# Kernel optimization log

Measured on AMD Instinct MI355X. Metric: run time of the kernel, lower is better.

## Reference

```python
import jax, jax.numpy as jnp
import numpy as np

CLS_W, BBOX_W, GIOU_W = 1.0, 5.0, 2.0
EPS = 1e-6


def _cxcywh_to_xyxy(b):
    cx, cy, w, h = b[..., 0], b[..., 1], b[..., 2], b[..., 3]
    return jnp.stack((cx - 0.5 * w, cy - 0.5 * h, cx + 0.5 * w, cy + 0.5 * h), axis=-1)


def _pairwise_giou(b1, b2):
    # b1: [N,4] xyxy, b2: [M,4] xyxy -> [N,M]
    b1 = b1[:, None, :]
    b2 = b2[None, :, :]
    iw = jnp.clip(jnp.minimum(b1[..., 2], b2[..., 2]) - jnp.maximum(b1[..., 0], b2[..., 0]), 0.0)
    ih = jnp.clip(jnp.minimum(b1[..., 3], b2[..., 3]) - jnp.maximum(b1[..., 1], b2[..., 1]), 0.0)
    inter = iw * ih
    area1 = (b1[..., 2] - b1[..., 0]) * (b1[..., 3] - b1[..., 1])
    area2 = (b2[..., 2] - b2[..., 0]) * (b2[..., 3] - b2[..., 1])
    union = area1 + area2 - inter
    iou = inter / (union + EPS)
    enc = (jnp.maximum(b1[..., 2], b2[..., 2]) - jnp.minimum(b1[..., 0], b2[..., 0])) * \
          (jnp.maximum(b1[..., 3], b2[..., 3]) - jnp.minimum(b1[..., 1], b2[..., 1])) + EPS
    return iou - (enc - union) / enc


def _cost_single(logits, boxes, tids, tboxes):
    # logits [N,C], boxes [N,4] cxcywh, tids [M] int, tboxes [M,4] cxcywh
    prob = jax.nn.softmax(logits, axis=-1)          # [N,C]
    cost_cls = -prob[:, tids]                        # [N,M] (num_classes>1: no id shift)
    cost_bbox = jnp.sum(jnp.abs(boxes[:, None, :] - tboxes[None, :, :]), axis=-1)  # L1 cdist
    giou = _pairwise_giou(_cxcywh_to_xyxy(boxes), _cxcywh_to_xyxy(tboxes))
    return CLS_W * cost_cls + BBOX_W * cost_bbox + GIOU_W * (-giou)


_batched_cost = jax.jit(jax.vmap(_cost_single))


def _lsa(cost):
    """Jonker-Volgenant style Hungarian, equivalent to scipy.linear_sum_assignment."""
    cost = np.asarray(cost, dtype=np.float64)
    transposed = cost.shape[0] > cost.shape[1]
    if transposed:
        cost = cost.T
    n, m = cost.shape
    INF = 1e18
    u = np.zeros(n + 1)
    v = np.zeros(m + 1)
    p = np.zeros(m + 1, dtype=np.int64)   # p[j] = row (1-based) matched to col j
    way = np.zeros(m + 1, dtype=np.int64)
    for i in range(1, n + 1):
        p[0] = i
        j0 = 0
        minv = np.full(m + 1, INF)
        used = np.zeros(m + 1, dtype=bool)
        while True:
            used[j0] = True
            i0 = p[j0]
            free = ~used[1:]
            cur = cost[i0 - 1] - u[i0] - v[1:]
            upd = free & (cur < minv[1:])
            minv[1:] = np.where(upd, cur, minv[1:])
            way[1:] = np.where(upd, j0, way[1:])
            cand = np.where(free, minv[1:], INF)
            j1 = int(np.argmin(cand)) + 1
            delta = cand[j1 - 1]
            u[p[used]] += delta
            v[used] -= delta
            minv[1:] = np.where(free, minv[1:] - delta, minv[1:])
            j0 = j1
            if p[j0] == 0:
                break
        while j0:
            j1 = way[j0]
            p[j0] = p[j1]
            j0 = j1
    col4row = np.zeros(n, dtype=np.int64)
    for j in range(1, m + 1):
        if p[j] > 0:
            col4row[p[j] - 1] = j - 1
    if transposed:
        order = np.argsort(col4row, kind='stable').astype(np.int64)
        return col4row[order], order
    return np.arange(n, dtype=np.int64), col4row


def setup_inputs() -> dict:
    key = jax.random.key(0)
    k1, k2, k3, k4 = jax.random.split(key, 4)
    B, N, C, M = 64, 900, 91, 128
    return {
        "pred_logits": jax.random.normal(k1, (B, N, C), dtype=jnp.float32),
        "pred_boxes": jax.random.uniform(k2, (B, N, 4), dtype=jnp.float32),
        "tgt_labels": jax.random.randint(k3, (B, M), 0, C, dtype=jnp.int64),
        "tgt_boxes": jax.random.uniform(k4, (B, M, 4), dtype=jnp.float32),
    }


def reference(pred_logits, pred_boxes, tgt_labels, tgt_boxes):
    # Batched cost matrix on accelerator, then per-image assignment on host
    C = _batched_cost(pred_logits, pred_boxes, tgt_labels, tgt_boxes)  # [B,N,M]
    Cn = np.asarray(C)
    rows, cols = [], []
    for b in range(Cn.shape[0]):
        r, c = _lsa(Cn[b])
        rows.append(r)
        cols.append(c)
    return jnp.asarray(np.stack(rows)), jnp.asarray(np.stack(cols))
```

## Files before the change

kernel.cpp:

```cpp
#include <hip/hip_runtime.h>
#include <hip/hip_bf16.h>
#include <float.h>

#define BB 64
#define NN 900
#define CC 91
#define MM 128
#define BIG 1e18
#define DINF __builtin_huge_val()
#define NSLOT 15
#define LAST_VALID 4
#define TPB_C 128

__global__ __launch_bounds__(TPB_C) void cost_kernel(
    const float* __restrict__ logits,
    const float* __restrict__ boxes,
    const int*   __restrict__ tlabels,
    const float* __restrict__ tboxes,
    float* __restrict__ costT)
{
    const int b   = blockIdx.y;
    const int p0  = blockIdx.x * TPB_C;
    const int cnt = min(TPB_C, NN - p0);
    const int tid = threadIdx.x;

    __shared__ float s_lg[TPB_C * CC];
    __shared__ float s_tb[MM][4];
    __shared__ int   s_tl[MM];

    {
        s_tl[tid] = tlabels[b * MM + tid];
        const float4 tb4 = ((const float4*)tboxes)[(size_t)b * MM + tid];
        s_tb[tid][0] = tb4.x; s_tb[tid][1] = tb4.y;
        s_tb[tid][2] = tb4.z; s_tb[tid][3] = tb4.w;
    }
    {
        const float* gbase = logits + ((size_t)b * NN + p0) * CC;
        const int total = cnt * CC;
        const int n4 = total >> 2;
        for (int k = tid; k < n4; k += TPB_C)
            ((float4*)s_lg)[k] = ((const float4*)gbase)[k];
        for (int k = (n4 << 2) + tid; k < total; k += TPB_C)
            s_lg[k] = gbase[k];
    }
    __syncthreads();
    if (tid >= cnt) return;

    const float* lg = s_lg + tid * CC;
    float mx = -INFINITY;
    for (int c = 0; c < CC; ++c) mx = fmaxf(mx, lg[c]);
    float ssum = 0.f;
    for (int c = 0; c < CC; ++c) ssum += expf(lg[c] - mx);

    const float4 bx4 = ((const float4*)boxes)[(size_t)b * NN + p0 + tid];
    const float cx = bx4.x, cy = bx4.y, w = bx4.z, h = bx4.w;
    const float px0 = cx - 0.5f * w, py0 = cy - 0.5f * h;
    const float px1 = cx + 0.5f * w, py1 = cy + 0.5f * h;
    const float parea = (px1 - px0) * (py1 - py0);

    float* outp = costT + (size_t)b * MM * NN + p0 + tid;
    for (int j = 0; j < MM; ++j) {
        const float tcx = s_tb[j][0], tcy = s_tb[j][1], tw = s_tb[j][2], th = s_tb[j][3];
        float l1 = ((fabsf(cx - tcx) + fabsf(cy - tcy)) + fabsf(w - tw)) + fabsf(h - th);
        const float tx0 = tcx - 0.5f * tw, ty0 = tcy - 0.5f * th;
        const float tx1 = tcx + 0.5f * tw, ty1 = tcy + 0.5f * th;
        float iw = fminf(px1, tx1) - fmaxf(px0, tx0); iw = fmaxf(iw, 0.f);
        float ih = fminf(py1, ty1) - fmaxf(py0, ty0); ih = fmaxf(ih, 0.f);
        const float inter = iw * ih;
        const float tarea = (tx1 - tx0) * (ty1 - ty0);
        const float uni   = parea + tarea - inter;
        const float iou   = inter / (uni + 1e-6f);
        const float enc   = (fmaxf(px1, tx1) - fminf(px0, tx0)) *
                            (fmaxf(py1, ty1) - fminf(py0, ty0)) + 1e-6f;
        const float giou  = iou - (enc - uni) / enc;
        const float pcls  = expf(lg[s_tl[j]] - mx) / ssum;
        const float cost  = (1.0f * (-pcls) + 5.0f * l1) + 2.0f * (-giou);
        outp[(size_t)j * NN] = cost;
    }
}

template<int CTRL, int ROW_MASK>
__device__ __forceinline__ unsigned dpp_min_u32_step(unsigned x) {
    const unsigned m = (unsigned)__builtin_amdgcn_update_dpp((int)x, (int)x, CTRL, ROW_MASK, 0xF, false);
    return m < x ? m : x;
}
__device__ __forceinline__ unsigned wave_min_u32(unsigned x) {
    x = dpp_min_u32_step<0xB1,  0xF>(x);
    x = dpp_min_u32_step<0x4E,  0xF>(x);
    x = dpp_min_u32_step<0x141, 0xF>(x);
    x = dpp_min_u32_step<0x140, 0xF>(x);
    x = dpp_min_u32_step<0x142, 0xA>(x);
    x = dpp_min_u32_step<0x143, 0xC>(x);
    return (unsigned)__builtin_amdgcn_readlane((int)x, 63);
}
__device__ __forceinline__ int d_hi(double d) { return (int)(__double_as_longlong(d) >> 32); }
__device__ __forceinline__ int d_lo(double d) { return (int)__double_as_longlong(d); }
__device__ __forceinline__ double mk_d(int hi, int lo) {
    return __longlong_as_double(((long long)hi << 32) | (unsigned long long)(unsigned)lo);
}

__global__ __launch_bounds__(64) void lsa_kernel(
    const float* __restrict__ costT,
    int* __restrict__ out)
{
    const int b    = blockIdx.x;
    const int lane = threadIdx.x;

    __shared__ double s_u[MM + 1];
    __shared__ int    s_p[NN + 1];
    __shared__ int    s_c4r[MM];
    __shared__ int    s_spill[3 * (NN + 2)];

    double v[NSLOT], minv[NSLOT];
    unsigned pay[NSLOT], pay_base[NSLOT];
    float  cv[NSLOT];

    for (int j = lane; j <= NN; j += 64) s_p[j] = 0;
    for (int i = lane; i <= MM; i += 64) s_u[i] = 0.0;
    #pragma unroll
    for (int s = 0; s < NSLOT; ++s) {
        v[s] = 0.0;
        pay_base[s] = ((unsigned)(s * 64 + lane + 1) << 18);
        pay[s] = pay_base[s];
    }
    __syncthreads();

    const float* cb = costT + (size_t)b * MM * NN;

    #pragma unroll
    for (int s = 0; s < NSLOT; ++s) {
        const bool valid = (s < NSLOT - 1) || (lane < LAST_VALID);
        cv[s] = valid ? cb[s * 64 + lane] : 0.f;
    }

    for (int i = 1; i <= MM; ++i) {
        unsigned used_mask = 0;
        #pragma unroll
        for (int s = 0; s < NSLOT; ++s) minv[s] = BIG;

        int T = 0;
        int curj0 = 0;
        int curi0 = i;
        int curway = 0;
        int nspill = 0;
        double ui0 = 0.0;
        int my_j0 = -1, my_i0 = 0, my_way = 0;

        while (true) {
            if (T < 63) {
                if (lane == T) { my_j0 = curj0; my_i0 = curi0; my_way = curway; }
            } else {
                if (lane == 0) {
                    s_spill[3 * nspill]     = curj0;
                    s_spill[3 * nspill + 1] = curi0;
                    s_spill[3 * nspill + 2] = curway;
                }
                ++nspill;
            }
            if (curj0 > 0) {
                const int jp = curj0 - 1;
                if ((jp & 63) == lane) used_mask |= 1u << (jp >> 6);
            }

            const unsigned pay_or = (unsigned)curj0 << 8;
            #pragma unroll
            for (int s = 0; s < NSLOT; ++s) {
                const bool valid = (s < NSLOT - 1) || (lane < LAST_VALID);
                const bool fr = valid && !((used_mask >> s) & 1u);
                const double cur = ((double)cv[s] - ui0) - v[s];
                const bool imp = fr && (cur < minv[s]);
                if (imp) { minv[s] = cur; pay[s] = pay_base[s] | pay_or; }
            }

            double n1v[8]; unsigned n1p[8];
            #pragma unroll
            for (int s = 0; s < 8; ++s) {
                const int a = 2 * s, c = 2 * s + 1;
                double va = minv[a]; unsigned pa = pay[a];
                if (c < NSLOT) { if (minv[c] < va) { va = minv[c]; pa = pay[c]; } }
                n1v[s] = va; n1p[s] = pa;
            }
            double n2v[4]; unsigned n2p[4];
            #pragma unroll
            for (int s = 0; s < 4; ++s) {
                double va = n1v[2*s]; unsigned pa = n1p[2*s];
                if (n1v[2*s+1] < va) { va = n1v[2*s+1]; pa = n1p[2*s+1]; }
                n2v[s] = va; n2p[s] = pa;
            }
            double n3v[2]; unsigned n3p[2];
            #pragma unroll
            for (int s = 0; s < 2; ++s) {
                double va = n2v[2*s]; unsigned pa = n2p[2*s];
                if (n2v[2*s+1] < va) { va = n2v[2*s+1]; pa = n2p[2*s+1]; }
                n3v[s] = va; n3p[s] = pa;
            }
            double bv = n3v[0]; unsigned bpay = n3p[0];
            if (n3v[1] < bv) { bv = n3v[1]; bpay = n3p[1]; }

            const double bvn = bv + 0.0;
            const int hi = d_hi(bvn);
            const int sm = hi >> 31;
            const unsigned th = (unsigned)(hi ^ (sm | 0x80000000));
            const unsigned minhi = wave_min_u32(th);

            const unsigned long long hit = __ballot(th == minhi);
            unsigned wpay; double delta;
            if (__builtin_popcountll(hit) == 1) {
                const int src = (int)__builtin_ctzll(hit);
                wpay  = (unsigned)__builtin_amdgcn_readlane((int)bpay, src);
                delta = mk_d(__builtin_amdgcn_readlane(hi, src),
                             __builtin_amdgcn_readlane(d_lo(bvn), src));
            } else {
                const unsigned tl = (unsigned)(d_lo(bvn) ^ sm);
                const unsigned minlo = wave_min_u32((th == minhi) ? tl : 0xFFFFFFFFu);
                const bool full = (th == minhi) && (tl == minlo);
                wpay = wave_min_u32(full ? bpay : 0xFFFFFFFFu);
                const int src = (int)__builtin_ctzll(__ballot(full));
                delta = mk_d(__builtin_amdgcn_readlane(hi, src),
                             __builtin_amdgcn_readlane(d_lo(bvn), src));
            }
            const int j1   = (int)(wpay >> 18);
            const int way1 = (int)((wpay >> 8) & 0x3FF);
            const int pj1  = (int)(wpay & 0xFF);

            double ui_next = 0.0;
            if (pj1 != 0) {
                const float* crow = cb + (size_t)(pj1 - 1) * NN;
                #pragma unroll
                for (int s = 0; s < NSLOT; ++s) {
                    const bool valid = (s < NSLOT - 1) || (lane < LAST_VALID);
                    if (valid) cv[s] = crow[s * 64 + lane];
                }
                ui_next = s_u[pj1];
            }

            if (T < 63) {
                if (lane <= T) s_u[my_i0] += delta;
            } else {
                if (lane == 0) s_u[i] += delta;
                double uval[NSLOT];
                #pragma unroll
                for (int s = 0; s < NSLOT; ++s) {
                    const bool valid = (s < NSLOT - 1) || (lane < LAST_VALID);
                    if (valid && ((used_mask >> s) & 1u))
                        uval[s] = s_u[pay_base[s] & 0xFF];
                }
                #pragma unroll
                for (int s = 0; s < NSLOT; ++s) {
                    const bool valid = (s < NSLOT - 1) || (lane < LAST_VALID);
                    if (valid && ((used_mask >> s) & 1u))
                        s_u[pay_base[s] & 0xFF] = uval[s] + delta;
                }
            }
            #pragma unroll
            for (int s = 0; s < NSLOT; ++s) {
                const bool valid = (s < NSLOT - 1) || (lane < LAST_VALID);
                if (valid) {
                    const bool ub = (used_mask >> s) & 1u;
                    v[s]    = ub ? v[s] - delta : v[s];
                    minv[s] = ub ? DINF : minv[s] - delta;
                }
            }

            if (pj1 == 0) {
                int ja = j1, jb = way1;
                const int cap = (T < 63) ? T : 62;
                while (jb != 0) {
                    int np, nw;
                    const unsigned long long bal = __ballot(lane <= cap && my_j0 == jb);
                    if (bal != 0) {
                        const int src = (int)__builtin_ctzll(bal);
                        np = __builtin_amdgcn_readlane(my_i0, src);
                        nw = __builtin_amdgcn_readlane(my_way, src);
                    } else {
                        np = 0; nw = 0;
                        for (int k = 0; k < nspill; ++k) {
                            if (s_spill[3 * k] == jb) {
                                np = s_spill[3 * k + 1];
                                nw = s_spill[3 * k + 2];
                                break;
                            }
                        }
                    }
                    if (lane == 0) s_p[ja] = np;
                    ja = jb; jb = nw;
                }
                if (lane == 0) s_p[ja] = i;
                break;
            }
            curj0 = j1; curi0 = pj1; curway = way1; ui0 = ui_next; ++T;
        }

        #pragma unroll
        for (int s = 0; s < NSLOT; ++s) {
            const bool valid = (s < NSLOT - 1) || (lane < LAST_VALID);
            if (valid) {
                const int j = s * 64 + lane + 1;
                pay_base[s] = ((unsigned)j << 18) | (unsigned)s_p[j];
            }
        }
        if (i < MM) {
            const float* crow = cb + (size_t)i * NN;
            #pragma unroll
            for (int s = 0; s < NSLOT; ++s) {
                const bool valid = (s < NSLOT - 1) || (lane < LAST_VALID);
                if (valid) cv[s] = crow[s * 64 + lane];
            }
        }
    }

    for (int j = 1 + lane; j <= NN; j += 64) {
        const int pj = s_p[j];
        if (pj > 0) s_c4r[pj - 1] = j - 1;
    }
    __syncthreads();

    for (int t = lane; t < MM; t += 64) {
        const int val = s_c4r[t];
        int rank = 0;
        for (int q = 0; q < MM; ++q) rank += (s_c4r[q] < val);
        out[(size_t)b * MM + rank] = val;
        out[(size_t)BB * MM + (size_t)b * MM + rank] = t;
    }
}

extern "C" void kernel_launch(void* const* d_in, const int* in_sizes, int n_in,
                              void* d_out, int out_size, void* d_ws, size_t ws_size,
                              hipStream_t stream) {
    const float* logits  = (const float*)d_in[0];
    const float* boxes   = (const float*)d_in[1];
    const int*   tlabels = (const int*)d_in[2];
    const float* tboxes  = (const float*)d_in[3];
    int*   out   = (int*)d_out;
    float* costT = (float*)d_ws;

    dim3 g1((NN + TPB_C - 1) / TPB_C, BB);
    cost_kernel<<<g1, TPB_C, 0, stream>>>(logits, boxes, tlabels, tboxes, costT);
    lsa_kernel<<<BB, 64, 0, stream>>>(costT, out);
}
```

Baseline: 435.9 us.

## Split cost computation into softmax-stats pass and per-target fill kernel

Replaces the single cost kernel with two kernels. The first computes per-prediction softmax max and sum. The second launches one block per (target, image) and writes coalesced float4 rows of the transposed cost matrix, gathering the needed logit directly from global memory. This aims to expose more parallelism and give coalesced writes, at the cost of an extra launch, extra workspace and scattered logit gathers. It falls back to the old kernel if the workspace is too small.

```diff
diff --git a/kernel.cpp b/kernel.cpp
--- a/kernel.cpp
+++ b/kernel.cpp
@@ -12,11 +12,95 @@
 #define LAST_VALID 4
 #define TPB_C 128
 
-__global__ __launch_bounds__(TPB_C) void cost_kernel(
+__global__ __launch_bounds__(TPB_C) void stats_kernel(
     const float* __restrict__ logits,
+    float* __restrict__ stats)
+{
+    const int b   = blockIdx.y;
+    const int p0  = blockIdx.x * TPB_C;
+    const int cnt = min(TPB_C, NN - p0);
+    const int tid = threadIdx.x;
+
+    __shared__ float s_lg[TPB_C * CC];
+
+    {
+        const float* gbase = logits + ((size_t)b * NN + p0) * CC;
+        const int total = cnt * CC;
+        const int n4 = total >> 2;
+        for (int k = tid; k < n4; k += TPB_C)
+            ((float4*)s_lg)[k] = ((const float4*)gbase)[k];
+        for (int k = (n4 << 2) + tid; k < total; k += TPB_C)
+            s_lg[k] = gbase[k];
+    }
+    __syncthreads();
+    if (tid >= cnt) return;
+
+    const float* lg = s_lg + tid * CC;
+    float mx = -INFINITY;
+    for (int c = 0; c < CC; ++c) mx = fmaxf(mx, lg[c]);
+    float ssum = 0.f;
+    for (int c = 0; c < CC; ++c) ssum += expf(lg[c] - mx);
+
+    ((float2*)stats)[(size_t)b * NN + p0 + tid] = make_float2(mx, ssum);
+}
+
+__global__ __launch_bounds__(256) void fill_kernel(
     const float* __restrict__ boxes,
     const int*   __restrict__ tlabels,
     const float* __restrict__ tboxes,
+    const float* __restrict__ stats,
+    const float* __restrict__ logits,
+    float* __restrict__ costT)
+{
+    const int j = blockIdx.x;
+    const int b = blockIdx.y;
+    const int t = threadIdx.x;
+    if (t >= NN / 4) return;
+    const int p4 = t * 4;
+
+    const int    tl = tlabels[b * MM + j];
+    const float4 tb = ((const float4*)tboxes)[(size_t)b * MM + j];
+    const float tcx = tb.x, tcy = tb.y, tw = tb.z, th = tb.w;
+    const float tx0 = tcx - 0.5f * tw, ty0 = tcy - 0.5f * th;
+    const float tx1 = tcx + 0.5f * tw, ty1 = tcy + 0.5f * th;
+    const float tarea = (tx1 - tx0) * (ty1 - ty0);
+
+    const float4* bx4 = (const float4*)boxes + (size_t)b * NN + p4;
+    const float4  s01 = ((const float4*)stats)[((size_t)b * NN + p4) >> 1];
+    const float4  s23 = ((const float4*)stats)[(((size_t)b * NN + p4) >> 1) + 1];
+    const float   smx[4] = {s01.x, s01.z, s23.x, s23.z};
+    const float   ssm[4] = {s01.y, s01.w, s23.y, s23.w};
+
+    float res[4];
+    #pragma unroll
+    for (int k = 0; k < 4; ++k) {
+        const float4 bx = bx4[k];
+        const float cx = bx.x, cy = bx.y, w = bx.z, h = bx.w;
+        const float px0 = cx - 0.5f * w, py0 = cy - 0.5f * h;
+        const float px1 = cx + 0.5f * w, py1 = cy + 0.5f * h;
+        const float parea = (px1 - px0) * (py1 - py0);
+
+        float l1 = ((fabsf(cx - tcx) + fabsf(cy - tcy)) + fabsf(w - tw)) + fabsf(h - th);
+        float iw = fminf(px1, tx1) - fmaxf(px0, tx0); iw = fmaxf(iw, 0.f);
+        float ih = fminf(py1, ty1) - fmaxf(py0, ty0); ih = fmaxf(ih, 0.f);
+        const float inter = iw * ih;
+        const float uni   = parea + tarea - inter;
+        const float iou   = inter / (uni + 1e-6f);
+        const float enc   = (fmaxf(px1, tx1) - fminf(px0, tx0)) *
+                            (fmaxf(py1, ty1) - fminf(py0, ty0)) + 1e-6f;
+        const float giou  = iou - (enc - uni) / enc;
+
+        const float lgt  = logits[((size_t)b * NN + p4 + k) * CC + tl];
+        const float pcls = expf(lgt - smx[k]) / ssm[k];
+        res[k] = (1.0f * (-pcls) + 5.0f * l1) + 2.0f * (-giou);
+    }
+    ((float4*)(costT + (size_t)(b * MM + j) * NN))[t] =
+        make_float4(res[0], res[1], res[2], res[3]);
+}
+
+__global__ __launch_bounds__(TPB_C) void cost_kernel(
+    const float* __restrict__ logits, const float* __restrict__ boxes,
+    const int* __restrict__ tlabels, const float* __restrict__ tboxes,
     float* __restrict__ costT)
 {
     const int b   = blockIdx.y;
@@ -334,7 +418,18 @@
     int*   out   = (int*)d_out;
     float* costT = (float*)d_ws;
 
-    dim3 g1((NN + TPB_C - 1) / TPB_C, BB);
-    cost_kernel<<<g1, TPB_C, 0, stream>>>(logits, boxes, tlabels, tboxes, costT);
+    const size_t costT_bytes = (size_t)BB * MM * NN * 4;
+    const size_t stats_bytes = (size_t)BB * NN * 2 * 4;
+
+    if (ws_size >= costT_bytes + stats_bytes) {
+        float* stats = (float*)((char*)d_ws + costT_bytes);
+        dim3 gs((NN + TPB_C - 1) / TPB_C, BB);
+        stats_kernel<<<gs, TPB_C, 0, stream>>>(logits, stats);
+        dim3 gf(MM, BB);
+        fill_kernel<<<gf, 256, 0, stream>>>(boxes, tlabels, tboxes, stats, logits, costT);
+    } else {
+        dim3 g1((NN + TPB_C - 1) / TPB_C, BB);
+        cost_kernel<<<g1, TPB_C, 0, stream>>>(logits, boxes, tlabels, tboxes, costT);
+    }
     lsa_kernel<<<BB, 64, 0, stream>>>(costT, out);
 }
```

Result: no change. 437.3 us (+0.3%).
